# Optimization experiments

Measured on AMD Instinct MI355X. Metric: run time of the kernel, lower is better.

The kernel has to match this reference:

```python
import jax, jax.numpy as jnp
import numpy as np

TAU = 20.0        # LIFNeuron default tau
THRESHOLD = 1.0   # LIFNeuron default threshold
RESET = 0.0       # LIFNeuron default reset
DT = 1.0          # SpikingNeuralNetwork dt
ALPHA = DT / TAU

B, T, I, H, O = 256, 128, 512, 1024, 512


def setup_inputs() -> dict:
    key = jax.random.key(0)
    ks = jax.random.split(key, 6)
    def w(k, shape, fan_in):
        return (jax.random.normal(k, shape, jnp.float32) / np.sqrt(fan_in)).astype(jnp.float32)
    return {
        "x":  jax.random.normal(ks[0], (B, T, I), jnp.float32),
        "We": w(ks[1], (I, H), I), "be": jnp.zeros((H,), jnp.float32),
        "W1": w(ks[2], (H, H), H), "b1": jnp.zeros((H,), jnp.float32),
        "W2": w(ks[3], (H, H), H), "b2": jnp.zeros((H,), jnp.float32),
        "Wo": w(ks[4], (H, O), H), "bo": jnp.zeros((O,), jnp.float32),
    }


def _lif(v, inp):
    # v += (-v + inp) * dt/tau; spike = (v >= thr); v = v*(1-spike) + reset*spike
    v = v + (inp - v) * ALPHA
    spike = (v >= THRESHOLD).astype(v.dtype)
    v = v * (1.0 - spike) + RESET * spike
    return v, spike


def reference(x, We, be, W1, b1, W2, b2, Wo, bo):
    b, t, _ = x.shape
    h_dim = We.shape[1]
    o_dim = Wo.shape[1]

    def step(carry, xt):
        v1, v2, vo = carry
        h = jax.nn.relu(xt @ We + be)          # [B, H]
        v1, s1 = _lif(v1, h)                   # neuron 0 (only 2 of 3 neurons used: zip truncation)
        h = s1 @ W1 + b1
        v2, s2 = _lif(v2, h)                   # neuron 1
        h = s2 @ W2 + b2                       # last hidden layer: no neuron applied before output_layer
        vo, so = _lif(vo, h @ Wo + bo)         # output neuron
        return (v1, v2, vo), (s1, s2, so)

    init = (jnp.zeros((b, h_dim), x.dtype),
            jnp.zeros((b, h_dim), x.dtype),
            jnp.zeros((b, o_dim), x.dtype))
    _, (S1, S2, SO) = jax.lax.scan(step, init, jnp.swapaxes(x, 0, 1))  # time-major scan
    # output_spike at last timestep + full (detached) spike history, stacked over time
    return SO[-1], S1, S2, SO
```

## Files before the change

kernel.cpp:

```cpp
#include <hip/hip_runtime.h>
#include <cstdint>
#include <cstddef>

#define B_ 256
#define T_ 128
#define I_ 512
#define H_ 1024
#define O_ 512
static constexpr float ALPHA = 1.0f / 20.0f;
static constexpr float THR   = 1.0f;
static constexpr float S12   = 0.000244140625f;

typedef _Float16 f16;
typedef __attribute__((ext_vector_type(8))) _Float16 f16x8;
typedef __attribute__((ext_vector_type(4))) float f32x4;

__device__ inline void gload_lds16(const void* gsrc, void* ldsdst) {
    __builtin_amdgcn_global_load_lds(
        (const __attribute__((address_space(1))) unsigned int*)gsrc,
        (__attribute__((address_space(3))) unsigned int*)ldsdst, 16, 0, 0);
}

template<bool PERM_X, bool RELU>
__global__ __launch_bounds__(256)
void gemm128(const float* __restrict__ A, const float* __restrict__ Bw,
             const float* __restrict__ bias, float* __restrict__ C,
             int M, int N, int K) {
    constexpr int BM = 128, BN = 128, BK = 16, TM = 8, TN = 8;
    __shared__ float As[BK][BM];
    __shared__ float Bs[BK][BN + 4];

    const int tid = threadIdx.x;
    const int ntile = N / BN;
    const int bx = blockIdx.x % ntile;
    const int by = blockIdx.x / ntile;
    const int row0 = by * BM, col0 = bx * BN;
    const int tx = tid & 15;
    const int ty = tid >> 4;

    float acc[TM][TN] = {};

    for (int k0 = 0; k0 < K; k0 += BK) {
#pragma unroll
        for (int p = 0; p < 2; ++p) {
            int f = tid + p * 256;
            int r  = f >> 2;
            int kc = (f & 3) << 2;
            int m = row0 + r;
            const float* arow;
            if (PERM_X) {
                int t = m >> 8;
                int b = m & 255;
                arow = A + (size_t)(b * T_ + t) * K;
            } else {
                arow = A + (size_t)m * K;
            }
            float4 v = *reinterpret_cast<const float4*>(arow + k0 + kc);
            As[kc + 0][r] = v.x;
            As[kc + 1][r] = v.y;
            As[kc + 2][r] = v.z;
            As[kc + 3][r] = v.w;
        }
#pragma unroll
        for (int p = 0; p < 2; ++p) {
            int f = tid + p * 256;
            int r  = f >> 5;
            int nc = (f & 31) << 2;
            float4 v = *reinterpret_cast<const float4*>(Bw + (size_t)(k0 + r) * N + col0 + nc);
            *reinterpret_cast<float4*>(&Bs[r][nc]) = v;
        }
        __syncthreads();

#pragma unroll
        for (int k = 0; k < BK; ++k) {
            float a[TM], b[TN];
#pragma unroll
            for (int i = 0; i < TM; ++i) a[i] = As[k][ty * TM + i];
#pragma unroll
            for (int j = 0; j < TN; ++j) b[j] = Bs[k][tx * TN + j];
#pragma unroll
            for (int i = 0; i < TM; ++i)
#pragma unroll
                for (int j = 0; j < TN; ++j)
                    acc[i][j] += a[i] * b[j];
        }
        __syncthreads();
    }

#pragma unroll
    for (int i = 0; i < TM; ++i) {
        size_t m = (size_t)(row0 + ty * TM + i);
#pragma unroll
        for (int jj = 0; jj < TN; jj += 4) {
            int n = col0 + tx * TN + jj;
            float4 c4;
            float c0 = acc[i][jj + 0] + bias[n + 0];
            float c1 = acc[i][jj + 1] + bias[n + 1];
            float c2 = acc[i][jj + 2] + bias[n + 2];
            float c3 = acc[i][jj + 3] + bias[n + 3];
            if (RELU) {
                c0 = fmaxf(c0, 0.f); c1 = fmaxf(c1, 0.f);
                c2 = fmaxf(c2, 0.f); c3 = fmaxf(c3, 0.f);
            }
            c4.x = c0; c4.y = c1; c4.z = c2; c4.w = c3;
            *reinterpret_cast<float4*>(C + m * N + n) = c4;
        }
    }
}

template<bool SPLITX, bool PERM, bool RELU, bool WRITE_LAST, bool F16OUT>
__global__ __launch_bounds__(256, 2)
void gemm_lif(const float* __restrict__ A,
              const f16* __restrict__ Bhi, const f16* __restrict__ Blo,
              const float* __restrict__ bias,
              float* __restrict__ S, float* __restrict__ last_out,
              f16* __restrict__ Sf,
              int N, int K) {
    constexpr int BK = 32;
    constexpr int NBUF = SPLITX ? 4 : 3;
    constexpr int BUFSTR = NBUF * 4096;
    constexpr size_t SMEM = (2 * BUFSTR * 2 > 64 * 132 * 4)
                                ? (size_t)(2 * BUFSTR * 2)
                                : (size_t)(64 * 132 * 4);
    __shared__ __align__(16) char smem[SMEM];
    f16* sm = (f16*)smem;
    float (*Cs)[132] = (float (*)[132])smem;

    const int tid  = threadIdx.x;
    const int lane = tid & 63;
    const int w    = tid >> 6;
    const int wr   = w >> 1, wc = w & 1;
    const int ntile = N >> 7;
    const int bx = blockIdx.x % ntile;
    const int b  = blockIdx.x / ntile;
    const int col0 = bx << 7;

    f32x4 acc0[4][4], acc1[4][4];
#pragma unroll
    for (int mi = 0; mi < 4; ++mi)
#pragma unroll
        for (int ni = 0; ni < 4; ++ni) {
            acc0[mi][ni] = {0.f, 0.f, 0.f, 0.f};
            acc1[mi][ni] = {0.f, 0.f, 0.f, 0.f};
        }

    {
        f16* Ah0 = sm;
        f16* Bh0 = sm + 4096;
        f16* Bl0 = sm + 8192;
        f16* Al0 = sm + 12288;
#pragma unroll
        for (int p = 0; p < 2; ++p) {
            int chunk = w * 2 + p;
            int r  = chunk * 16 + (lane >> 2);
            int kq = lane & 3;
            size_t off = (size_t)(col0 + r) * K + kq * 8;
            gload_lds16(Bhi + off, Bh0 + chunk * 512);
            gload_lds16(Blo + off, Bl0 + chunk * 512);
        }
#pragma unroll
        for (int p = 0; p < 4; ++p) {
            int c = tid + p * 256;
            int r = c >> 3;
            int q = c & 7;
            const float* arow = PERM ? A + (size_t)(b * T_ + r) * K
                                     : A + (size_t)(r * B_ + b) * K;
            float4 v = *reinterpret_cast<const float4*>(arow + q * 4);
            union { f16 h[4]; uint2 u; } hi;
            hi.h[0] = (f16)v.x; hi.h[1] = (f16)v.y;
            hi.h[2] = (f16)v.z; hi.h[3] = (f16)v.w;
            *reinterpret_cast<uint2*>(&Ah0[r * BK + q * 4]) = hi.u;
            if (SPLITX) {
                union { f16 h[4]; uint2 u; } lo;
                lo.h[0] = (f16)((v.x - (float)hi.h[0]) * 4096.0f);
                lo.h[1] = (f16)((v.y - (float)hi.h[1]) * 4096.0f);
                lo.h[2] = (f16)((v.z - (float)hi.h[2]) * 4096.0f);
                lo.h[3] = (f16)((v.w - (float)hi.h[3]) * 4096.0f);
                *reinterpret_cast<uint2*>(&Al0[r * BK + q * 4]) = lo.u;
            }
        }
    }
    __syncthreads();

    const int NIT = K / BK;
    for (int it = 0; it < NIT; ++it) {
        const int cur = it & 1, nxt = cur ^ 1;
        const bool more = (it + 1 < NIT);
        const int k0n = (it + 1) * BK;

        f16* Ah_c = sm + cur * BUFSTR;
        f16* Bh_c = Ah_c + 4096;
        f16* Bl_c = Ah_c + 8192;
        f16* Al_c = Ah_c + 12288;
        f16* Ah_n = sm + nxt * BUFSTR;
        f16* Bh_n = Ah_n + 4096;
        f16* Bl_n = Ah_n + 8192;
        f16* Al_n = Ah_n + 12288;

        float4 a4[4];
        if (more) {
#pragma unroll
            for (int p = 0; p < 2; ++p) {
                int chunk = w * 2 + p;
                int r  = chunk * 16 + (lane >> 2);
                int kq = lane & 3;
                size_t off = (size_t)(col0 + r) * K + k0n + kq * 8;
                gload_lds16(Bhi + off, Bh_n + chunk * 512);
                gload_lds16(Blo + off, Bl_n + chunk * 512);
            }
#pragma unroll
            for (int p = 0; p < 4; ++p) {
                int c = tid + p * 256;
                int r = c >> 3;
                int q = c & 7;
                const float* arow = PERM ? A + (size_t)(b * T_ + r) * K
                                         : A + (size_t)(r * B_ + b) * K;
                a4[p] = *reinterpret_cast<const float4*>(arow + k0n + q * 4);
            }
        }

        {
            f16x8 ahi[4], alo[4];
#pragma unroll
            for (int mi = 0; mi < 4; ++mi) {
                int ar = (wr * 64 + mi * 16 + (lane & 15)) * BK + (lane >> 4) * 8;
                ahi[mi] = *reinterpret_cast<const f16x8*>(&Ah_c[ar]);
                if (SPLITX) alo[mi] = *reinterpret_cast<const f16x8*>(&Al_c[ar]);
            }
#pragma unroll
            for (int ni = 0; ni < 4; ++ni) {
                int br = (wc * 64 + ni * 16 + (lane & 15)) * BK + (lane >> 4) * 8;
                f16x8 bh = *reinterpret_cast<const f16x8*>(&Bh_c[br]);
                f16x8 bl = *reinterpret_cast<const f16x8*>(&Bl_c[br]);
#pragma unroll
                for (int mi = 0; mi < 4; ++mi) {
                    acc0[mi][ni] = __builtin_amdgcn_mfma_f32_16x16x32_f16(
                        ahi[mi], bh, acc0[mi][ni], 0, 0, 0);
                    acc1[mi][ni] = __builtin_amdgcn_mfma_f32_16x16x32_f16(
                        ahi[mi], bl, acc1[mi][ni], 0, 0, 0);
                    if (SPLITX)
                        acc1[mi][ni] = __builtin_amdgcn_mfma_f32_16x16x32_f16(
                            alo[mi], bh, acc1[mi][ni], 0, 0, 0);
                }
            }
        }

        if (more) {
#pragma unroll
            for (int p = 0; p < 4; ++p) {
                int c = tid + p * 256;
                int r = c >> 3;
                int q = c & 7;
                float4 v = a4[p];
                union { f16 h[4]; uint2 u; } hi;
                hi.h[0] = (f16)v.x; hi.h[1] = (f16)v.y;
                hi.h[2] = (f16)v.z; hi.h[3] = (f16)v.w;
                *reinterpret_cast<uint2*>(&Ah_n[r * BK + q * 4]) = hi.u;
                if (SPLITX) {
                    union { f16 h[4]; uint2 u; } lo;
                    lo.h[0] = (f16)((v.x - (float)hi.h[0]) * 4096.0f);
                    lo.h[1] = (f16)((v.y - (float)hi.h[1]) * 4096.0f);
                    lo.h[2] = (f16)((v.z - (float)hi.h[2]) * 4096.0f);
                    lo.h[3] = (f16)((v.w - (float)hi.h[3]) * 4096.0f);
                    *reinterpret_cast<uint2*>(&Al_n[r * BK + q * 4]) = lo.u;
                }
            }
        }
        __syncthreads();
    }

    float v = 0.f, s = 0.f;
    float* Sp = S + (size_t)b * N + col0 + (tid & 127);
    const size_t tstride = (size_t)B_ * N;

    if (wr == 0) {
#pragma unroll
        for (int ni = 0; ni < 4; ++ni) {
            int col = wc * 64 + ni * 16 + (lane & 15);
            float bv = bias[col0 + col];
#pragma unroll
            for (int mi = 0; mi < 4; ++mi) {
                int rowb = mi * 16 + ((lane >> 4) << 2);
#pragma unroll
                for (int r = 0; r < 4; ++r) {
                    float cv = acc0[mi][ni][r] + S12 * acc1[mi][ni][r] + bv;
                    if (RELU) cv = fmaxf(cv, 0.f);
                    Cs[rowb + r][col] = cv;
                }
            }
        }
    }
    __syncthreads();
    if (tid < 128) {
#pragma unroll 4
        for (int t = 0; t < 64; ++t) {
            float in = Cs[t][tid];
            v = v + (in - v) * ALPHA;
            bool sp = (v >= THR);
            s = sp ? 1.0f : 0.0f;
            Sp[(size_t)t * tstride] = s;
            if (F16OUT) Sf[((size_t)b * T_ + t) * N + col0 + tid] = (f16)s;
            v = sp ? 0.0f : v;
        }
    }
    __syncthreads();
    if (wr == 1) {
#pragma unroll
        for (int ni = 0; ni < 4; ++ni) {
            int col = wc * 64 + ni * 16 + (lane & 15);
            float bv = bias[col0 + col];
#pragma unroll
            for (int mi = 0; mi < 4; ++mi) {
                int rowb = mi * 16 + ((lane >> 4) << 2);
#pragma unroll
                for (int r = 0; r < 4; ++r) {
                    float cv = acc0[mi][ni][r] + S12 * acc1[mi][ni][r] + bv;
                    if (RELU) cv = fmaxf(cv, 0.f);
                    Cs[rowb + r][col] = cv;
                }
            }
        }
    }
    __syncthreads();
    if (tid < 128) {
#pragma unroll 4
        for (int t = 64; t < 128; ++t) {
            float in = Cs[t - 64][tid];
            v = v + (in - v) * ALPHA;
            bool sp = (v >= THR);
            s = sp ? 1.0f : 0.0f;
            Sp[(size_t)t * tstride] = s;
            if (F16OUT) Sf[((size_t)b * T_ + t) * N + col0 + tid] = (f16)s;
            v = sp ? 0.0f : v;
        }
        if (WRITE_LAST) last_out[(size_t)b * N + col0 + tid] = s;
    }
}

template<bool WRITE_LAST, bool F16OUT>
__global__ __launch_bounds__(256, 2)
void gemm_lif_h(const f16* __restrict__ Af,
                const f16* __restrict__ Bhi,
                const f16* __restrict__ Blo,
                const float* __restrict__ bias,
                float* __restrict__ S,
                float* __restrict__ last_out,
                f16* __restrict__ Sf,
                int N, int K) {
    constexpr int BK = 32;
    constexpr int BUFF = 3 * 4096;
    __shared__ __align__(16) char smem[2 * BUFF * 2];
    f16* sm = (f16*)smem;
    float (*Cs)[132] = (float (*)[132])smem;

    const int tid  = threadIdx.x;
    const int lane = tid & 63;
    const int w    = tid >> 6;
    const int wr   = w >> 1, wc = w & 1;
    const int ntile = N >> 7;
    const int bx = blockIdx.x % ntile;
    const int b  = blockIdx.x / ntile;
    const int col0 = bx << 7;
    const int sw = (((lane >> 4) ^ ((lane >> 1) & 3)) << 3);

    f32x4 acc0[4][4], acc1[4][4];
#pragma unroll
    for (int mi = 0; mi < 4; ++mi)
#pragma unroll
        for (int ni = 0; ni < 4; ++ni) {
            acc0[mi][ni] = {0.f, 0.f, 0.f, 0.f};
            acc1[mi][ni] = {0.f, 0.f, 0.f, 0.f};
        }

    const int r0   = (w * 2 + 0) * 16 + (lane >> 2);
    const int r1   = (w * 2 + 1) * 16 + (lane >> 2);
    const int kqs  = lane & 3;
    const int kqa0 = kqs ^ ((r0 >> 1) & 3);
    const int kqa1 = kqs ^ ((r1 >> 1) & 3);

    {
        size_t b0 = (size_t)(col0 + r0) * K + kqs * 8;
        size_t b1 = (size_t)(col0 + r1) * K + kqs * 8;
        size_t a0 = ((size_t)b * T_ + r0) * K + kqa0 * 8;
        size_t a1 = ((size_t)b * T_ + r1) * K + kqa1 * 8;
        gload_lds16(Af + a0,  sm + (w * 2 + 0) * 512);
        gload_lds16(Af + a1,  sm + (w * 2 + 1) * 512);
        gload_lds16(Bhi + b0, sm + 4096 + (w * 2 + 0) * 512);
        gload_lds16(Bhi + b1, sm + 4096 + (w * 2 + 1) * 512);
        gload_lds16(Blo + b0, sm + 8192 + (w * 2 + 0) * 512);
        gload_lds16(Blo + b1, sm + 8192 + (w * 2 + 1) * 512);
    }
    __syncthreads();

    const int NIT = K / BK;
    for (int it = 0; it < NIT; ++it) {
        f16* cur = sm + (it & 1) * BUFF;
        if (it + 1 < NIT) {
            f16* nb = sm + ((it + 1) & 1) * BUFF;
            int k0n = (it + 1) * BK;
            size_t b0 = (size_t)(col0 + r0) * K + k0n + kqs * 8;
            size_t b1 = (size_t)(col0 + r1) * K + k0n + kqs * 8;
            size_t a0 = ((size_t)b * T_ + r0) * K + k0n + kqa0 * 8;
            size_t a1 = ((size_t)b * T_ + r1) * K + k0n + kqa1 * 8;
            gload_lds16(Af + a0,  nb + (w * 2 + 0) * 512);
            gload_lds16(Af + a1,  nb + (w * 2 + 1) * 512);
            gload_lds16(Bhi + b0, nb + 4096 + (w * 2 + 0) * 512);
            gload_lds16(Bhi + b1, nb + 4096 + (w * 2 + 1) * 512);
            gload_lds16(Blo + b0, nb + 8192 + (w * 2 + 0) * 512);
            gload_lds16(Blo + b1, nb + 8192 + (w * 2 + 1) * 512);
        }

        f16x8 af[4];
#pragma unroll
        for (int mi = 0; mi < 4; ++mi)
            af[mi] = *reinterpret_cast<const f16x8*>(
                &cur[(wr * 64 + mi * 16 + (lane & 15)) * BK + sw]);
#pragma unroll
        for (int ni = 0; ni < 4; ++ni) {
            int br = (wc * 64 + ni * 16 + (lane & 15)) * BK + sw;
            f16x8 bh = *reinterpret_cast<const f16x8*>(&cur[4096 + br]);
            f16x8 bl = *reinterpret_cast<const f16x8*>(&cur[8192 + br]);
#pragma unroll
            for (int mi = 0; mi < 4; ++mi) {
                acc0[mi][ni] = __builtin_amdgcn_mfma_f32_16x16x32_f16(
                    af[mi], bh, acc0[mi][ni], 0, 0, 0);
                acc1[mi][ni] = __builtin_amdgcn_mfma_f32_16x16x32_f16(
                    af[mi], bl, acc1[mi][ni], 0, 0, 0);
            }
        }
        __syncthreads();
    }

    float v = 0.f, s = 0.f;
    float* Sp = S + (size_t)b * N + col0 + (tid & 127);
    const size_t tstride = (size_t)B_ * N;

    if (wr == 0) {
#pragma unroll
        for (int ni = 0; ni < 4; ++ni) {
            int col = wc * 64 + ni * 16 + (lane & 15);
            float bv = bias[col0 + col];
#pragma unroll
            for (int mi = 0; mi < 4; ++mi) {
                int rowb = mi * 16 + ((lane >> 4) << 2);
#pragma unroll
                for (int r = 0; r < 4; ++r)
                    Cs[rowb + r][col] = acc0[mi][ni][r] + S12 * acc1[mi][ni][r] + bv;
            }
        }
    }
    __syncthreads();
    if (tid < 128) {
#pragma unroll 4
        for (int t = 0; t < 64; ++t) {
            float in = Cs[t][tid];
            v = v + (in - v) * ALPHA;
            bool sp = (v >= THR);
            s = sp ? 1.0f : 0.0f;
            Sp[(size_t)t * tstride] = s;
            if (F16OUT) Sf[((size_t)b * T_ + t) * N + col0 + tid] = (f16)s;
            v = sp ? 0.0f : v;
        }
    }
    __syncthreads();
    if (wr == 1) {
#pragma unroll
        for (int ni = 0; ni < 4; ++ni) {
            int col = wc * 64 + ni * 16 + (lane & 15);
            float bv = bias[col0 + col];
#pragma unroll
            for (int mi = 0; mi < 4; ++mi) {
                int rowb = mi * 16 + ((lane >> 4) << 2);
#pragma unroll
                for (int r = 0; r < 4; ++r)
                    Cs[rowb + r][col] = acc0[mi][ni][r] + S12 * acc1[mi][ni][r] + bv;
            }
        }
    }
    __syncthreads();
    if (tid < 128) {
#pragma unroll 4
        for (int t = 64; t < 128; ++t) {
            float in = Cs[t - 64][tid];
            v = v + (in - v) * ALPHA;
            bool sp = (v >= THR);
            s = sp ? 1.0f : 0.0f;
            Sp[(size_t)t * tstride] = s;
            if (F16OUT) Sf[((size_t)b * T_ + t) * N + col0 + tid] = (f16)s;
            v = sp ? 0.0f : v;
        }
        if (WRITE_LAST) last_out[(size_t)b * N + col0 + tid] = s;
    }
}

__global__ __launch_bounds__(256)
void lif_scan(float* __restrict__ buf, int BH, float* __restrict__ last_out) {
    int j = blockIdx.x * 256 + threadIdx.x;
    if (j >= BH) return;
    float v = 0.f;
    float last = 0.f;
    for (int t = 0; t < T_; ++t) {
        size_t idx = (size_t)t * BH + j;
        float in = buf[idx];
        v = v + (in - v) * ALPHA;
        bool sp = (v >= THR);
        last = sp ? 1.0f : 0.0f;
        buf[idx] = last;
        v = sp ? 0.0f : v;
    }
    if (last_out) last_out[j] = last;
}

__global__ __launch_bounds__(256)
void make_wf2(const float* __restrict__ W2, const float* __restrict__ Wo,
              float* __restrict__ Wf) {
    __shared__ float w2s[64][33];
    __shared__ float wos[64][68];
    const int tid = threadIdx.x;
    const int ht = blockIdx.x >> 3, ot = blockIdx.x & 7;
    const int h0 = ht * 32, o0 = ot * 64;
    const int th = tid >> 3;
    const int to = tid & 7;

    double acc[8] = {0, 0, 0, 0, 0, 0, 0, 0};

    for (int k0 = 0; k0 < H_; k0 += 64) {
#pragma unroll
        for (int p = 0; p < 2; ++p) {
            int f = tid + p * 256;
            int i = f >> 4;
            int j4 = (f & 15) << 2;
            float4 v = *reinterpret_cast<const float4*>(
                W2 + (size_t)(h0 + i) * H_ + k0 + j4);
            w2s[j4 + 0][i] = v.x; w2s[j4 + 1][i] = v.y;
            w2s[j4 + 2][i] = v.z; w2s[j4 + 3][i] = v.w;
        }
#pragma unroll
        for (int p = 0; p < 4; ++p) {
            int f = tid + p * 256;
            int r = f >> 4;
            int c4 = (f & 15) << 2;
            float4 v = *reinterpret_cast<const float4*>(
                Wo + (size_t)(k0 + r) * O_ + o0 + c4);
            wos[r][c4 + 0] = v.x; wos[r][c4 + 1] = v.y;
            wos[r][c4 + 2] = v.z; wos[r][c4 + 3] = v.w;
        }
        __syncthreads();

#pragma unroll 8
        for (int k = 0; k < 64; ++k) {
            double a = (double)w2s[k][th];
#pragma unroll
            for (int j = 0; j < 8; ++j)
                acc[j] += a * (double)wos[k][to * 8 + j];
        }
        __syncthreads();
    }
#pragma unroll
    for (int j = 0; j < 8; ++j)
        Wf[(size_t)(h0 + th) * O_ + o0 + to * 8 + j] = (float)acc[j];
}

__global__ __launch_bounds__(256)
void make_bf(const float* __restrict__ Wo, const float* __restrict__ b2,
             const float* __restrict__ bo, float* __restrict__ bf) {
    int o = blockIdx.x * 256 + threadIdx.x;
    if (o >= O_) return;
    double acc = (double)bo[o];
    for (int h = 0; h < H_; ++h)
        acc += (double)b2[h] * (double)Wo[(size_t)h * O_ + o];
    bf[o] = (float)acc;
}

template<bool SWZ>
__global__ __launch_bounds__(256)
void split_w16(const float* __restrict__ W, f16* __restrict__ hi,
               f16* __restrict__ lo, int K, int N) {
    int idx = blockIdx.x * 256 + threadIdx.x;
    if (idx >= K * N) return;
    int n = idx / K;
    int ks = idx - n * K;
    int k = SWZ ? ((ks & ~31) | ((((ks >> 3) & 3) ^ ((n >> 1) & 3)) << 3) | (ks & 7))
                : ks;
    float wv = W[(size_t)k * N + n];
    f16 h0 = (f16)wv;
    float r = (wv - (float)h0) * 4096.0f;
    f16 h1 = (f16)r;
    hi[idx] = h0; lo[idx] = h1;
}

extern "C" void kernel_launch(void* const* d_in, const int* in_sizes, int n_in,
                              void* d_out, int out_size, void* d_ws, size_t ws_size,
                              hipStream_t stream) {
    const float* x  = (const float*)d_in[0];
    const float* We = (const float*)d_in[1];
    const float* be = (const float*)d_in[2];
    const float* W1 = (const float*)d_in[3];
    const float* b1 = (const float*)d_in[4];
    const float* W2 = (const float*)d_in[5];
    const float* b2 = (const float*)d_in[6];
    const float* Wo = (const float*)d_in[7];
    const float* bo = (const float*)d_in[8];

    float* out = (float*)d_out;
    float* so_last = out;
    float* S1 = out + (size_t)B_ * O_;
    float* S2 = S1 + (size_t)T_ * B_ * H_;
    float* SO = S2 + (size_t)T_ * B_ * H_;

    const int TB = T_ * B_;
    dim3 blk(256);

    const size_t MB = 1024 * 1024;
    const size_t off_weh = 0;
    const size_t off_wel = 1 * MB;
    const size_t off_w1h = 2 * MB;
    const size_t off_w1l = 4 * MB;
    const size_t off_wfh = 6 * MB;
    const size_t off_wfl = 7 * MB;
    const size_t off_bf  = 8 * MB;
    const size_t off_wf  = 8 * MB + 4096;
    const size_t off_s1f = 10 * MB + 4096;
    const size_t sz_s1f  = (size_t)T_ * B_ * H_ * 2;
    const size_t off_s2f = off_s1f + sz_s1f;
    const size_t need_hi = off_s2f + sz_s1f;

    const size_t m_off_weh = 0;
    const size_t m_off_wel = m_off_weh + (size_t)I_ * H_ * 2;
    const size_t m_off_w1h = m_off_wel + (size_t)I_ * H_ * 2;
    const size_t m_off_w1l = m_off_w1h + (size_t)H_ * H_ * 2;
    const size_t m_off_wf32 = m_off_w1l + (size_t)H_ * H_ * 2;
    const size_t m_off_bf   = m_off_wf32 + (size_t)H_ * O_ * 4;
    const size_t m_off_wfh  = m_off_bf + (size_t)O_ * 4;
    const size_t m_off_wfl  = m_off_wfh + (size_t)H_ * O_ * 2;
    const size_t need_mid   = m_off_wfl + (size_t)H_ * O_ * 2;

    if (ws_size >= need_hi) {
        char* ws = (char*)d_ws;
        f16*   weh = (f16*)(ws + off_weh);
        f16*   wel = (f16*)(ws + off_wel);
        f16*   w1h = (f16*)(ws + off_w1h);
        f16*   w1l = (f16*)(ws + off_w1l);
        f16*   wfh = (f16*)(ws + off_wfh);
        f16*   wfl = (f16*)(ws + off_wfl);
        float* bf  = (float*)(ws + off_bf);
        float* Wf  = (float*)(ws + off_wf);
        f16*   s1f = (f16*)(ws + off_s1f);
        f16*   s2f = (f16*)(ws + off_s2f);

        split_w16<false><<<dim3((I_ * H_ + 255) / 256), blk, 0, stream>>>(We, weh, wel, I_, H_);
        split_w16<true ><<<dim3((H_ * H_ + 255) / 256), blk, 0, stream>>>(W1, w1h, w1l, H_, H_);
        make_wf2<<<dim3(256), blk, 0, stream>>>(W2, Wo, Wf);
        make_bf<<<dim3(2), blk, 0, stream>>>(Wo, b2, bo, bf);
        split_w16<true ><<<dim3((H_ * O_ + 255) / 256), blk, 0, stream>>>(Wf, wfh, wfl, H_, O_);

        gemm_lif<true, true, true, false, true><<<dim3(B_ * (H_ / 128)), blk, 0, stream>>>(
            x, weh, wel, be, S1, nullptr, s1f, H_, I_);

        gemm_lif_h<false, true><<<dim3(B_ * (H_ / 128)), blk, 0, stream>>>(
            s1f, w1h, w1l, b1, S2, nullptr, s2f, H_, H_);

        gemm_lif_h<true, false><<<dim3(B_ * (O_ / 128)), blk, 0, stream>>>(
            s2f, wfh, wfl, bf, SO, so_last, nullptr, O_, H_);
    } else if (ws_size >= need_mid) {
        char* ws = (char*)d_ws;
        f16*   weh = (f16*)(ws + m_off_weh);
        f16*   wel = (f16*)(ws + m_off_wel);
        f16*   w1h = (f16*)(ws + m_off_w1h);
        f16*   w1l = (f16*)(ws + m_off_w1l);
        float* Wf  = (float*)(ws + m_off_wf32);
        float* bf  = (float*)(ws + m_off_bf);
        f16*   wfh = (f16*)(ws + m_off_wfh);
        f16*   wfl = (f16*)(ws + m_off_wfl);

        split_w16<false><<<dim3((I_ * H_ + 255) / 256), blk, 0, stream>>>(We, weh, wel, I_, H_);
        split_w16<false><<<dim3((H_ * H_ + 255) / 256), blk, 0, stream>>>(W1, w1h, w1l, H_, H_);
        make_wf2<<<dim3(256), blk, 0, stream>>>(W2, Wo, Wf);
        make_bf<<<dim3(2), blk, 0, stream>>>(Wo, b2, bo, bf);
        split_w16<false><<<dim3((H_ * O_ + 255) / 256), blk, 0, stream>>>(Wf, wfh, wfl, H_, O_);

        gemm_lif<true, true, true, false, false><<<dim3(B_ * (H_ / 128)), blk, 0, stream>>>(
            x, weh, wel, be, S1, nullptr, nullptr, H_, I_);
        gemm_lif<false, false, false, false, false><<<dim3(B_ * (H_ / 128)), blk, 0, stream>>>(
            S1, w1h, w1l, b1, S2, nullptr, nullptr, H_, H_);
        gemm_lif<false, false, false, true, false><<<dim3(B_ * (O_ / 128)), blk, 0, stream>>>(
            S2, wfh, wfl, bf, SO, so_last, nullptr, O_, H_);
    } else {
        float* Wf = (float*)d_ws;
        float* bf = Wf + (size_t)H_ * O_;
        gemm128<true, true><<<dim3((TB / 128) * (H_ / 128)), blk, 0, stream>>>(
            x, We, be, S1, TB, H_, I_);
        lif_scan<<<dim3((B_ * H_ + 255) / 256), blk, 0, stream>>>(S1, B_ * H_, nullptr);
        gemm128<false, false><<<dim3((TB / 128) * (H_ / 128)), blk, 0, stream>>>(
            S1, W1, b1, S2, TB, H_, H_);
        lif_scan<<<dim3((B_ * H_ + 255) / 256), blk, 0, stream>>>(S2, B_ * H_, nullptr);
        make_wf2<<<dim3(256), blk, 0, stream>>>(W2, Wo, Wf);
        make_bf<<<dim3(2), blk, 0, stream>>>(Wo, b2, bo, bf);
        gemm128<false, false><<<dim3((TB / 128) * (O_ / 128)), blk, 0, stream>>>(
            S2, Wf, bf, SO, TB, O_, H_);
        lif_scan<<<dim3((B_ * O_ + 255) / 256), blk, 0, stream>>>(SO, B_ * O_, so_last);
    }
}
```

Before: 582.2 us.

## Pre-split x into fp16 hi/lo and run layer 1 through async-LDS MFMA kernel

Adds a kernel that splits the fp32 input x into fp16 high and scaled-low halves, then runs the first layer through the gemm_lif_h path. That path uses global_load_lds double buffering and a third MFMA for the x_lo*W_hi term, with ReLU fused into the epilogue. The aim is to replace the older first-layer kernel, which reads fp32 x directly, with the faster direct-to-LDS pipeline. The cost is an extra pass over x (read fp32, write two fp16 copies), more workspace, and 50% more MFMAs in layer 1.

```diff
diff --git a/kernel.cpp b/kernel.cpp
--- a/kernel.cpp
+++ b/kernel.cpp
@@ -337,9 +337,10 @@
     }
 }
 
-template<bool WRITE_LAST, bool F16OUT>
+template<bool AX, bool RELU, bool WRITE_LAST, bool F16OUT>
 __global__ __launch_bounds__(256, 2)
 void gemm_lif_h(const f16* __restrict__ Af,
+                const f16* __restrict__ Alo_,
                 const f16* __restrict__ Bhi,
                 const f16* __restrict__ Blo,
                 const float* __restrict__ bias,
@@ -348,8 +349,12 @@
                 f16* __restrict__ Sf,
                 int N, int K) {
     constexpr int BK = 32;
-    constexpr int BUFF = 3 * 4096;
-    __shared__ __align__(16) char smem[2 * BUFF * 2];
+    constexpr int NB = AX ? 4 : 3;
+    constexpr int BUFF = NB * 4096;
+    constexpr size_t SMEM = (2 * (size_t)BUFF * 2 > 64 * 132 * 4)
+                                ? (size_t)(2 * BUFF * 2)
+                                : (size_t)(64 * 132 * 4);
+    __shared__ __align__(16) char smem[SMEM];
     f16* sm = (f16*)smem;
     float (*Cs)[132] = (float (*)[132])smem;
 
@@ -389,6 +394,10 @@
         gload_lds16(Bhi + b1, sm + 4096 + (w * 2 + 1) * 512);
         gload_lds16(Blo + b0, sm + 8192 + (w * 2 + 0) * 512);
         gload_lds16(Blo + b1, sm + 8192 + (w * 2 + 1) * 512);
+        if (AX) {
+            gload_lds16(Alo_ + a0, sm + 12288 + (w * 2 + 0) * 512);
+            gload_lds16(Alo_ + a1, sm + 12288 + (w * 2 + 1) * 512);
+        }
     }
     __syncthreads();
 
@@ -408,13 +417,19 @@
             gload_lds16(Bhi + b1, nb + 4096 + (w * 2 + 1) * 512);
             gload_lds16(Blo + b0, nb + 8192 + (w * 2 + 0) * 512);
             gload_lds16(Blo + b1, nb + 8192 + (w * 2 + 1) * 512);
-        }
-
-        f16x8 af[4];
-#pragma unroll
-        for (int mi = 0; mi < 4; ++mi)
-            af[mi] = *reinterpret_cast<const f16x8*>(
-                &cur[(wr * 64 + mi * 16 + (lane & 15)) * BK + sw]);
+            if (AX) {
+                gload_lds16(Alo_ + a0, nb + 12288 + (w * 2 + 0) * 512);
+                gload_lds16(Alo_ + a1, nb + 12288 + (w * 2 + 1) * 512);
+            }
+        }
+
+        f16x8 af[4], al[4];
+#pragma unroll
+        for (int mi = 0; mi < 4; ++mi) {
+            int ar = (wr * 64 + mi * 16 + (lane & 15)) * BK + sw;
+            af[mi] = *reinterpret_cast<const f16x8*>(&cur[ar]);
+            if (AX) al[mi] = *reinterpret_cast<const f16x8*>(&cur[12288 + ar]);
+        }
 #pragma unroll
         for (int ni = 0; ni < 4; ++ni) {
             int br = (wc * 64 + ni * 16 + (lane & 15)) * BK + sw;
@@ -426,6 +441,9 @@
                     af[mi], bh, acc0[mi][ni], 0, 0, 0);
                 acc1[mi][ni] = __builtin_amdgcn_mfma_f32_16x16x32_f16(
                     af[mi], bl, acc1[mi][ni], 0, 0, 0);
+                if (AX)
+                    acc1[mi][ni] = __builtin_amdgcn_mfma_f32_16x16x32_f16(
+                        al[mi], bh, acc1[mi][ni], 0, 0, 0);
             }
         }
         __syncthreads();
@@ -444,8 +462,11 @@
             for (int mi = 0; mi < 4; ++mi) {
                 int rowb = mi * 16 + ((lane >> 4) << 2);
 #pragma unroll
-                for (int r = 0; r < 4; ++r)
-                    Cs[rowb + r][col] = acc0[mi][ni][r] + S12 * acc1[mi][ni][r] + bv;
+                for (int r = 0; r < 4; ++r) {
+                    float cv = acc0[mi][ni][r] + S12 * acc1[mi][ni][r] + bv;
+                    if (RELU) cv = fmaxf(cv, 0.f);
+                    Cs[rowb + r][col] = cv;
+                }
             }
         }
     }
@@ -472,8 +493,11 @@
             for (int mi = 0; mi < 4; ++mi) {
                 int rowb = mi * 16 + ((lane >> 4) << 2);
 #pragma unroll
-                for (int r = 0; r < 4; ++r)
-                    Cs[rowb + r][col] = acc0[mi][ni][r] + S12 * acc1[mi][ni][r] + bv;
+                for (int r = 0; r < 4; ++r) {
+                    float cv = acc0[mi][ni][r] + S12 * acc1[mi][ni][r] + bv;
+                    if (RELU) cv = fmaxf(cv, 0.f);
+                    Cs[rowb + r][col] = cv;
+                }
             }
         }
     }
@@ -491,6 +515,22 @@
         }
         if (WRITE_LAST) last_out[(size_t)b * N + col0 + tid] = s;
     }
+}
+
+__global__ __launch_bounds__(256)
+void split_x16(const float* __restrict__ X, f16* __restrict__ hi,
+               f16* __restrict__ lo, int total4) {
+    int i = blockIdx.x * 256 + threadIdx.x;
+    if (i >= total4) return;
+    float4 v = reinterpret_cast<const float4*>(X)[i];
+    union { f16 h[4]; uint2 u; } H, L;
+    H.h[0] = (f16)v.x; H.h[1] = (f16)v.y; H.h[2] = (f16)v.z; H.h[3] = (f16)v.w;
+    L.h[0] = (f16)((v.x - (float)H.h[0]) * 4096.0f);
+    L.h[1] = (f16)((v.y - (float)H.h[1]) * 4096.0f);
+    L.h[2] = (f16)((v.z - (float)H.h[2]) * 4096.0f);
+    L.h[3] = (f16)((v.w - (float)H.h[3]) * 4096.0f);
+    reinterpret_cast<uint2*>(hi)[i] = H.u;
+    reinterpret_cast<uint2*>(lo)[i] = L.u;
 }
 
 __global__ __launch_bounds__(256)
@@ -612,41 +652,88 @@
     dim3 blk(256);
 
     const size_t MB = 1024 * 1024;
-    const size_t off_weh = 0;
-    const size_t off_wel = 1 * MB;
-    const size_t off_w1h = 2 * MB;
-    const size_t off_w1l = 4 * MB;
-    const size_t off_wfh = 6 * MB;
-    const size_t off_wfl = 7 * MB;
-    const size_t off_bf  = 8 * MB;
-    const size_t off_wf  = 8 * MB + 4096;
-    const size_t off_s1f = 10 * MB + 4096;
-    const size_t sz_s1f  = (size_t)T_ * B_ * H_ * 2;
-    const size_t off_s2f = off_s1f + sz_s1f;
-    const size_t need_hi = off_s2f + sz_s1f;
-
-    const size_t m_off_weh = 0;
-    const size_t m_off_wel = m_off_weh + (size_t)I_ * H_ * 2;
-    const size_t m_off_w1h = m_off_wel + (size_t)I_ * H_ * 2;
-    const size_t m_off_w1l = m_off_w1h + (size_t)H_ * H_ * 2;
-    const size_t m_off_wf32 = m_off_w1l + (size_t)H_ * H_ * 2;
-    const size_t m_off_bf   = m_off_wf32 + (size_t)H_ * O_ * 4;
-    const size_t m_off_wfh  = m_off_bf + (size_t)O_ * 4;
-    const size_t m_off_wfl  = m_off_wfh + (size_t)H_ * O_ * 2;
-    const size_t need_mid   = m_off_wfl + (size_t)H_ * O_ * 2;
-
-    if (ws_size >= need_hi) {
+    const size_t sz_x   = (size_t)B_ * T_ * I_ * 2;
+    const size_t sz_s1f = (size_t)T_ * B_ * H_ * 2;
+
+    const size_t a_weh = 0;
+    const size_t a_wel = 1 * MB;
+    const size_t a_w1h = 2 * MB;
+    const size_t a_w1l = 4 * MB;
+    const size_t a_wfh = 6 * MB;
+    const size_t a_wfl = 7 * MB;
+    const size_t a_bf  = 8 * MB;
+    const size_t a_wf  = 8 * MB + 4096;
+    const size_t a_xhi = 10 * MB + 4096;
+    const size_t a_xlo = a_xhi + sz_x;
+    const size_t a_s1f = a_xlo + sz_x;
+    const size_t a_s2f = a_s1f + sz_s1f;
+    const size_t need_A = a_s2f + sz_s1f;
+
+    const size_t b_weh = 0;
+    const size_t b_wel = 1 * MB;
+    const size_t b_w1h = 2 * MB;
+    const size_t b_w1l = 4 * MB;
+    const size_t b_wfh = 6 * MB;
+    const size_t b_wfl = 7 * MB;
+    const size_t b_bf  = 8 * MB;
+    const size_t b_wf  = 8 * MB + 4096;
+    const size_t b_s1f = 10 * MB + 4096;
+    const size_t b_s2f = b_s1f + sz_s1f;
+    const size_t need_B = b_s2f + sz_s1f;
+
+    const size_t m_weh = 0;
+    const size_t m_wel = m_weh + (size_t)I_ * H_ * 2;
+    const size_t m_w1h = m_wel + (size_t)I_ * H_ * 2;
+    const size_t m_w1l = m_w1h + (size_t)H_ * H_ * 2;
+    const size_t m_wf  = m_w1l + (size_t)H_ * H_ * 2;
+    const size_t m_bf  = m_wf + (size_t)H_ * O_ * 4;
+    const size_t m_wfh = m_bf + (size_t)O_ * 4;
+    const size_t m_wfl = m_wfh + (size_t)H_ * O_ * 2;
+    const size_t need_mid = m_wfl + (size_t)H_ * O_ * 2;
+
+    if (ws_size >= need_A) {
         char* ws = (char*)d_ws;
-        f16*   weh = (f16*)(ws + off_weh);
-        f16*   wel = (f16*)(ws + off_wel);
-        f16*   w1h = (f16*)(ws + off_w1h);
-        f16*   w1l = (f16*)(ws + off_w1l);
-        f16*   wfh = (f16*)(ws + off_wfh);
-        f16*   wfl = (f16*)(ws + off_wfl);
-        float* bf  = (float*)(ws + off_bf);
-        float* Wf  = (float*)(ws + off_wf);
-        f16*   s1f = (f16*)(ws + off_s1f);
-        f16*   s2f = (f16*)(ws + off_s2f);
+        f16*   weh = (f16*)(ws + a_weh);
+        f16*   wel = (f16*)(ws + a_wel);
+        f16*   w1h = (f16*)(ws + a_w1h);
+        f16*   w1l = (f16*)(ws + a_w1l);
+        f16*   wfh = (f16*)(ws + a_wfh);
+        f16*   wfl = (f16*)(ws + a_wfl);
+        float* bf  = (float*)(ws + a_bf);
+        float* Wf  = (float*)(ws + a_wf);
+        f16*   xhi = (f16*)(ws + a_xhi);
+        f16*   xlo = (f16*)(ws + a_xlo);
+        f16*   s1f = (f16*)(ws + a_s1f);
+        f16*   s2f = (f16*)(ws + a_s2f);
+
+        split_x16<<<dim3((B_ * T_ * I_ / 4 + 255) / 256), blk, 0, stream>>>(
+            x, xhi, xlo, B_ * T_ * I_ / 4);
+        split_w16<true><<<dim3((I_ * H_ + 255) / 256), blk, 0, stream>>>(We, weh, wel, I_, H_);
+        split_w16<true><<<dim3((H_ * H_ + 255) / 256), blk, 0, stream>>>(W1, w1h, w1l, H_, H_);
+        make_wf2<<<dim3(256), blk, 0, stream>>>(W2, Wo, Wf);
+        make_bf<<<dim3(2), blk, 0, stream>>>(Wo, b2, bo, bf);
+        split_w16<true><<<dim3((H_ * O_ + 255) / 256), blk, 0, stream>>>(Wf, wfh, wfl, H_, O_);
+
+        gemm_lif_h<true, true, false, true><<<dim3(B_ * (H_ / 128)), blk, 0, stream>>>(
+            xhi, xlo, weh, wel, be, S1, nullptr, s1f, H_, I_);
+
+        gemm_lif_h<false, false, false, true><<<dim3(B_ * (H_ / 128)), blk, 0, stream>>>(
+            s1f, nullptr, w1h, w1l, b1, S2, nullptr, s2f, H_, H_);
+
+        gemm_lif_h<false, false, true, false><<<dim3(B_ * (O_ / 128)), blk, 0, stream>>>(
+            s2f, nullptr, wfh, wfl, bf, SO, so_last, nullptr, O_, H_);
+    } else if (ws_size >= need_B) {
+        char* ws = (char*)d_ws;
+        f16*   weh = (f16*)(ws + b_weh);
+        f16*   wel = (f16*)(ws + b_wel);
+        f16*   w1h = (f16*)(ws + b_w1h);
+        f16*   w1l = (f16*)(ws + b_w1l);
+        f16*   wfh = (f16*)(ws + b_wfh);
+        f16*   wfl = (f16*)(ws + b_wfl);
+        float* bf  = (float*)(ws + b_bf);
+        float* Wf  = (float*)(ws + b_wf);
+        f16*   s1f = (f16*)(ws + b_s1f);
+        f16*   s2f = (f16*)(ws + b_s2f);
 
         split_w16<false><<<dim3((I_ * H_ + 255) / 256), blk, 0, stream>>>(We, weh, wel, I_, H_);
         split_w16<true ><<<dim3((H_ * H_ + 255) / 256), blk, 0, stream>>>(W1, w1h, w1l, H_, H_);
@@ -656,22 +743,20 @@
 
         gemm_lif<true, true, true, false, true><<<dim3(B_ * (H_ / 128)), blk, 0, stream>>>(
             x, weh, wel, be, S1, nullptr, s1f, H_, I_);
-
-        gemm_lif_h<false, true><<<dim3(B_ * (H_ / 128)), blk, 0, stream>>>(
-            s1f, w1h, w1l, b1, S2, nullptr, s2f, H_, H_);
-
-        gemm_lif_h<true, false><<<dim3(B_ * (O_ / 128)), blk, 0, stream>>>(
-            s2f, wfh, wfl, bf, SO, so_last, nullptr, O_, H_);
+        gemm_lif_h<false, false, false, true><<<dim3(B_ * (H_ / 128)), blk, 0, stream>>>(
+            s1f, nullptr, w1h, w1l, b1, S2, nullptr, s2f, H_, H_);
+        gemm_lif_h<false, false, true, false><<<dim3(B_ * (O_ / 128)), blk, 0, stream>>>(
+            s2f, nullptr, wfh, wfl, bf, SO, so_last, nullptr, O_, H_);
     } else if (ws_size >= need_mid) {
         char* ws = (char*)d_ws;
-        f16*   weh = (f16*)(ws + m_off_weh);
-        f16*   wel = (f16*)(ws + m_off_wel);
-        f16*   w1h = (f16*)(ws + m_off_w1h);
-        f16*   w1l = (f16*)(ws + m_off_w1l);
-        float* Wf  = (float*)(ws + m_off_wf32);
-        float* bf  = (float*)(ws + m_off_bf);
-        f16*   wfh = (f16*)(ws + m_off_wfh);
-        f16*   wfl = (f16*)(ws + m_off_wfl);
+        f16*   weh = (f16*)(ws + m_weh);
+        f16*   wel = (f16*)(ws + m_wel);
+        f16*   w1h = (f16*)(ws + m_w1h);
+        f16*   w1l = (f16*)(ws + m_w1l);
+        float* Wf  = (float*)(ws + m_wf);
+        float* bf  = (float*)(ws + m_bf);
+        f16*   wfh = (f16*)(ws + m_wfh);
+        f16*   wfl = (f16*)(ws + m_wfl);
 
         split_w16<false><<<dim3((I_ * H_ + 255) / 256), blk, 0, stream>>>(We, weh, wel, I_, H_);
         split_w16<false><<<dim3((H_ * H_ + 255) / 256), blk, 0, stream>>>(W1, w1h, w1l, H_, H_);
```

New measurement: 605.1 us. 1.04x slower.
